# Kernel tuning notes

Measured on AMD Instinct MI355X. Metric: run time of the kernel, lower is better.

Reference implementation:

```python
import jax, jax.numpy as jnp
import numpy as np

T, B, D = 1024, 8, 1024
H, DH = 16, 64
EPS = 1e-12  # F.normalize eps

def _xavier(key, shape):
    fan_in, fan_out = shape[1], shape[0]
    a = float(np.sqrt(6.0 / (fan_in + fan_out)))
    return jax.random.uniform(key, shape, jnp.float32, -a, a)

def setup_inputs() -> dict:
    key = jax.random.key(0)
    ks = jax.random.split(key, 6)
    return {
        "x": jax.random.normal(ks[0], (T, B, D), jnp.float32),
        "S0": jnp.zeros((B, H, DH, DH), jnp.float32),
        "W_q": _xavier(ks[1], (D, D)),
        "W_k": _xavier(ks[2], (D, D)),
        "W_v": _xavier(ks[3], (D, D)),
        "W_alpha": _xavier(ks[4], (D, D)),
        "b_alpha": jnp.full((D,), 2.0, jnp.float32),
        "W_beta": _xavier(ks[5], (D, D)),
        "b_beta": jnp.zeros((D,), jnp.float32),
    }

def _l2norm(v):
    n = jnp.linalg.norm(v, axis=-1, keepdims=True)
    return v / jnp.maximum(n, EPS)

def reference(x, S0, W_q, W_k, W_v, W_alpha, b_alpha, W_beta, b_beta):
    t, b, d = x.shape
    h, dh = d // DH, DH
    xf = x.reshape(t * b, d)
    q = _l2norm((xf @ W_q.T).reshape(t, b, h, dh))
    k = _l2norm((xf @ W_k.T).reshape(t, b, h, dh))
    v = (xf @ W_v.T).reshape(t, b, h, dh)
    # per-head scalar gates: mean over head dim of sigmoid projections
    alpha = jax.nn.sigmoid(xf @ W_alpha.T + b_alpha).reshape(t, b, h, dh).mean(-1)  # [T,B,H]
    beta = jax.nn.sigmoid(xf @ W_beta.T + b_beta).reshape(t, b, h, dh).mean(-1)     # [T,B,H]

    def step(S, inp):
        qt, kt, vt, at, bt = inp  # [B,H,dh], [B,H,dh], [B,H,dh], [B,H], [B,H]
        a = at[:, :, None, None]
        be = bt[:, :, None, None]
        Sk = jnp.einsum('bhde,bhe->bhd', S, kt)                 # S @ k
        erase = Sk[..., :, None] * kt[..., None, :]             # (S k) k^T
        write = vt[..., :, None] * kt[..., None, :]             # v k^T
        S = a * (S - be * erase) + be * write
        out = jnp.einsum('bhde,bhe->bhd', S, qt).reshape(-1, d)  # [B,D]
        return S, out

    S_final, outs = jax.lax.scan(step, S0, (q, k, v, alpha, beta))
    return outs, S_final
```

## Files before the change

kernel.cpp:

```cpp
#include <hip/hip_runtime.h>
#include <hip/hip_bf16.h>
#include <math.h>

#define T_DIM 1024
#define B_DIM 8
#define D_DIM 1024
#define H_DIM 16
#define DH 64
#define M_ROWS 8192
#define N_COLS 5120
#define K_DIM 1024
#define PAD 72

typedef __attribute__((ext_vector_type(8))) short short8;
typedef __attribute__((ext_vector_type(4))) float floatx4;

static __device__ __forceinline__ unsigned short f2bf(float f){
    unsigned int u = __float_as_uint(f);
    u += 0x7fff + ((u >> 16) & 1);
    return (unsigned short)(u >> 16);
}
static __device__ __forceinline__ float sigf(float x){
    return 1.f / (1.f + __expf(-x));
}

#define DPPADD(x, ctrl) ((x) + __int_as_float(__builtin_amdgcn_update_dpp(0, __float_as_int(x), (ctrl), 0xF, 0xF, true)))
static __device__ __forceinline__ float red16(float x){
    x = DPPADD(x, 0xB1); x = DPPADD(x, 0x4E); x = DPPADD(x, 0x141); x = DPPADD(x, 0x140); return x;
}

__global__ void cvt_bf16(const float* __restrict__ src, unsigned short* __restrict__ dst, int n4){
    int i = blockIdx.x*blockDim.x + threadIdx.x;
    int stride = gridDim.x*blockDim.x;
    for (; i < n4; i += stride){
        float4 f = ((const float4*)src)[i];
        ushort4 o;
        o.x = f2bf(f.x); o.y = f2bf(f.y); o.z = f2bf(f.z); o.w = f2bf(f.w);
        ((ushort4*)dst)[i] = o;
    }
}

__global__ void cvt_w(const float* __restrict__ w0, const float* __restrict__ w1,
                      const float* __restrict__ w2, const float* __restrict__ w3,
                      const float* __restrict__ w4, unsigned short* __restrict__ dst){
    int i = blockIdx.x*blockDim.x + threadIdx.x;
    int seg = i >> 18;
    int off = i & 262143;
    const float* src = (seg==0)?w0:(seg==1)?w1:(seg==2)?w2:(seg==3)?w3:w4;
    float4 f = ((const float4*)src)[off];
    ushort4 o;
    o.x = f2bf(f.x); o.y = f2bf(f.y); o.z = f2bf(f.z); o.w = f2bf(f.w);
    ((ushort4*)dst)[i] = o;
}

#define GLD16(g, l) __builtin_amdgcn_global_load_lds(                         \
    (const __attribute__((address_space(1))) void*)(g),                       \
    (__attribute__((address_space(3))) void*)(l), 16, 0, 0)

#define SBAR() do { asm volatile("" ::: "memory"); __builtin_amdgcn_s_barrier(); asm volatile("" ::: "memory"); } while(0)

#define STAGE(slot, kk) do {                                                  \
    GLD16(pA0 + (kk)*32, &As[slot][tid*8]);                                   \
    GLD16(pA1 + (kk)*32, &As[slot][4096 + tid*8]);                            \
    GLD16(pB0 + (kk)*32, &Bs[slot][tid*8]);                                   \
    GLD16(pB1 + (kk)*32, &Bs[slot][4096 + tid*8]); } while(0)

#define READ_FRAGS(aF, bF, slot) do {                                         \
    aF[0] = *(const short8*)&As[slot][rowA];                                  \
    _Pragma("unroll")                                                         \
    for (int n = 0; n < 4; ++n) bF[n] = *(const short8*)&Bs[slot][rowB + n*512]; \
    _Pragma("unroll")                                                         \
    for (int m = 1; m < 8; ++m) aF[m] = *(const short8*)&As[slot][rowA + m*512]; \
} while(0)

#define MFMA_ALL(aF, bF) do {                                                 \
    __builtin_amdgcn_s_setprio(1);                                            \
    _Pragma("unroll")                                                         \
    for (int m = 0; m < 8; ++m)                                               \
        _Pragma("unroll")                                                     \
        for (int n = 0; n < 4; ++n)                                           \
            acc[m][n] = __builtin_amdgcn_mfma_f32_16x16x32_bf16(aF[m], bF[n], acc[m][n], 0,0,0); \
    __builtin_amdgcn_s_setprio(0);                                            \
} while(0)

__global__ __launch_bounds__(512, 2) void gemm_bt(const unsigned short* __restrict__ A,
                                                  const unsigned short* __restrict__ B,
                                                  unsigned char* __restrict__ KQV,
                                                  float* __restrict__ G,
                                                  const float* __restrict__ b_alpha,
                                                  const float* __restrict__ b_beta){
    __shared__ unsigned short As[4][8192];
    __shared__ unsigned short Bs[4][8192];
    const int tid = threadIdx.x;

    const int bid = blockIdx.y * 20 + blockIdx.x;
    const int xcd = bid & 7, idx = bid >> 3;
    const int ch = idx / 20, w20 = idx % 20;
    const int rowBase = (xcd*4 + (w20 & 3)) * 256;
    const int colBase = (ch*5 + (w20 >> 2)) * 256;

    const int l = tid & 63, l15 = l & 15, quad = l >> 4;
    const int wv = tid >> 6, wr = wv >> 2, wc = wv & 3;

    const int fk   = (quad ^ ((l15 >> 1) & 3)) * 8;
    const int rowA = (wr*128 + l15)*32 + fk;
    const int rowB = (wc*64  + l15)*32 + fk;

    const int kOff = ((tid & 3) ^ ((tid >> 3) & 3)) * 8;
    const unsigned short* pA0 = A + (size_t)(rowBase + (tid >> 2)) * K_DIM + kOff;
    const unsigned short* pA1 = pA0 + (size_t)128 * K_DIM;
    const unsigned short* pB0 = B + (size_t)(colBase + (tid >> 2)) * K_DIM + kOff;
    const unsigned short* pB1 = pB0 + (size_t)128 * K_DIM;

    floatx4 acc[8][4] = {};
    short8 aF0[8], bF0[4], aF1[8], bF1[4];

    STAGE(0, 0); STAGE(1, 1); STAGE(2, 2);
    asm volatile("s_waitcnt vmcnt(8)" ::: "memory");
    SBAR();
    READ_FRAGS(aF0, bF0, 0);
    asm volatile("s_waitcnt vmcnt(4)" ::: "memory");
    SBAR();

    for (int kk = 0; kk < 32; kk += 2){
        READ_FRAGS(aF1, bF1, (kk+1)&3);
        if (kk < 29) STAGE((kk+3)&3, kk+3);
        MFMA_ALL(aF0, bF0);
        if (kk < 29) asm volatile("s_waitcnt vmcnt(4)" ::: "memory");
        SBAR();
        if (kk+1 < 31) READ_FRAGS(aF0, bF0, (kk+2)&3);
        if (kk+1 < 29) STAGE((kk+4)&3, kk+4);
        MFMA_ALL(aF1, bF1);
        if (kk+1 < 29)       asm volatile("s_waitcnt vmcnt(4)" ::: "memory");
        else if (kk+1 == 29) asm volatile("s_waitcnt vmcnt(0)" ::: "memory");
        SBAR();
    }

    const int gcol = colBase + wc*64;
    const int seg  = gcol >> 10;
    const int rbw  = rowBase + wr*128 + quad*4;
    if (seg < 2){
        const int h = (gcol >> 6) & 15;
        const int segOff = (seg == 0) ? 128 : 0;
        #pragma unroll
        for (int m = 0; m < 8; ++m){
            #pragma unroll
            for (int r = 0; r < 4; ++r){
                float ss = acc[m][0][r]*acc[m][0][r] + acc[m][1][r]*acc[m][1][r]
                         + acc[m][2][r]*acc[m][2][r] + acc[m][3][r]*acc[m][3][r];
                ss = red16(ss);
                const float rn = 1.f / fmaxf(sqrtf(ss), 1e-12f);
                const int row = rbw + m*16 + r;
                const size_t rec = (size_t)((row & 7)*16 + h)*1024 + (row >> 3);
                unsigned short* rp = (unsigned short*)(KQV + rec*512 + segOff);
                #pragma unroll
                for (int n = 0; n < 4; ++n)
                    rp[n*16 + l15] = f2bf(acc[m][n][r] * rn);
            }
        }
    } else if (seg == 2){
        const int h = (gcol >> 6) & 15;
        #pragma unroll
        for (int m = 0; m < 8; ++m){
            #pragma unroll
            for (int r = 0; r < 4; ++r){
                const int row = rbw + m*16 + r;
                const size_t rec = (size_t)((row & 7)*16 + h)*1024 + (row >> 3);
                float* vp = (float*)(KQV + rec*512 + 256);
                #pragma unroll
                for (int n = 0; n < 4; ++n)
                    vp[n*16 + l15] = acc[m][n][r];
            }
        }
    } else {
        const int isBeta = (seg == 4) ? 1 : 0;
        const float* bias = isBeta ? b_beta : b_alpha;
        const int gcol0 = gcol - (isBeta ? 4096 : 3072);
        const int hh = gcol0 >> 6;
        float bj[4];
        #pragma unroll
        for (int n = 0; n < 4; ++n) bj[n] = bias[gcol0 + n*16 + l15];
        #pragma unroll
        for (int m = 0; m < 8; ++m){
            #pragma unroll
            for (int r = 0; r < 4; ++r){
                float sum = 0.f;
                #pragma unroll
                for (int n = 0; n < 4; ++n) sum += sigf(acc[m][n][r] + bj[n]);
                sum = red16(sum);
                if (l15 == 0){
                    const int row = rbw + m*16 + r;
                    const int tt = row >> 3, bb = row & 7;
                    G[(((size_t)(bb*16 + hh)*1024 + tt))*2 + isBeta] = sum * (1.f/64.f);
                }
            }
        }
    }
}

__global__ __launch_bounds__(256) void phasea(const unsigned char* __restrict__ KQV,
                                              const float* __restrict__ G,
                                              unsigned short* __restrict__ Wtg,
                                              unsigned short* __restrict__ Ng,
                                              float* __restrict__ rg){
    __shared__ unsigned short sKa[64*PAD], sQa[64*PAD];
    __shared__ float sAB[128];
    __shared__ float sKK[4096];
    __shared__ float sR[64], sRi[64];

    const int unitIdx = blockIdx.x;
    const int bh = unitIdx >> 4, c = unitIdx & 15;
    const int tid = threadIdx.x;
    const int w = tid>>6, l = tid&63, l15 = l&15, quad = l>>4;
    const unsigned char* gRec = KQV + ((size_t)bh*1024 + c*64)*512;

    #pragma unroll
    for (int it=0; it<2; ++it){
        int flat = it*256 + tid, t = flat>>3, i8 = flat&7;
        float4 kv = *(const float4*)(gRec + t*512 + i8*16);
        float4 qv = *(const float4*)(gRec + t*512 + 128 + i8*16);
        *(float4*)&sKa[t*PAD + i8*8] = kv;
        *(float4*)&sQa[t*PAD + i8*8] = qv;
    }
    if (tid < 64){
        float2 ab = *(const float2*)(G + ((size_t)bh*1024 + c*64 + tid)*2);
        sAB[tid*2] = ab.x; sAB[tid*2+1] = ab.y;
    }
    __syncthreads();
    if (tid < 64){
        float p = sAB[tid*2];
        #pragma unroll
        for (int off=1; off<64; off<<=1){
            float y = __shfl_up(p, off);
            if (tid >= off) p *= y;
        }
        sR[tid] = p; sRi[tid] = 1.f/p;
    }
    __syncthreads();

    {
        const int isQK = w >> 1;
        const int tmb = (w & 1)*2;
        floatx4 acc[2][4] = {};
        #pragma unroll
        for (int ks=0; ks<2; ++ks){
            short8 aA[2]; short8 bB[4];
            #pragma unroll
            for (int i=0;i<2;++i)
                aA[i] = *(const short8*)&((isQK? sQa : sKa)[((tmb+i)*16 + l15)*PAD + ks*32 + quad*8]);
            #pragma unroll
            for (int j2=0;j2<4;++j2)
                bB[j2] = *(const short8*)&sKa[(j2*16 + l15)*PAD + ks*32 + quad*8];
            #pragma unroll
            for (int i=0;i<2;++i)
                #pragma unroll
                for (int j2=0;j2<4;++j2)
                    acc[i][j2] = __builtin_amdgcn_mfma_f32_16x16x32_bf16(aA[i], bB[j2], acc[i][j2], 0,0,0);
        }
        #pragma unroll
        for (int i=0;i<2;++i){
            #pragma unroll
            for (int j2=0;j2<4;++j2){
                #pragma unroll
                for (int r=0;r<4;++r){
                    int t = (tmb+i)*16 + quad*4 + r;
                    int s = j2*16 + l15;
                    float ratio = sR[t]*sRi[s];
                    if (!isQK){
                        sKK[t*64+s] = (s < t) ? sAB[t*2+1]*ratio*acc[i][j2][r] : 0.f;
                    } else {
                        float nv = (s <= t) ? ratio*acc[i][j2][r] : 0.f;
                        Ng[(size_t)unitIdx*4096 + t*64 + s] = f2bf(nv);
                    }
                }
            }
        }
    }
    __syncthreads();

    if (tid < 64){
        const int s = tid;
        float X[64];
        X[0] = (s == 0) ? 1.f : 0.f;
        #pragma unroll
        for (int t=1; t<64; ++t){
            float a0 = 0.f, a1 = 0.f;
            const float* row = &sKK[t*64];
            int r = 0;
            #pragma unroll
            for (; r+4 <= t; r += 4){
                float4 cv = *(const float4*)&row[r];
                a0 += cv.x * X[r];
                a1 += cv.y * X[r+1];
                a0 += cv.z * X[r+2];
                a1 += cv.w * X[r+3];
            }
            #pragma unroll
            for (; r+1 < t; r += 2){
                a0 += row[r]   * X[r];
                a1 += row[r+1] * X[r+1];
            }
            if (r < t) a0 += row[r] * X[r];
            X[t] = (s == t) ? 1.f : -(a0+a1);
        }
        const float be = sAB[s*2+1];
        #pragma unroll
        for (int t=0; t<64; ++t)
            Wtg[(size_t)unitIdx*4096 + t*64 + s] = f2bf(X[t]*be);
        rg[(size_t)unitIdx*64 + s] = sR[s];
    }
}

__global__ __launch_bounds__(512) void chunk_scan(const unsigned char* __restrict__ KQV,
                                                  const unsigned short* __restrict__ Wtg,
                                                  const unsigned short* __restrict__ Ng,
                                                  const float* __restrict__ rg,
                                                  const float* __restrict__ S0g,
                                                  float* __restrict__ out){
    __shared__ unsigned short sK[64*PAD], sQ[64*PAD], sWt[64*PAD];
    __shared__ unsigned short sN[2][64*PAD];
    __shared__ unsigned short sUt[32*PAD];
    __shared__ unsigned short sKtU[64*PAD];
    __shared__ unsigned short sS0b[32*PAD];
    __shared__ float sr[2][64];

    const int bh = blockIdx.x & 127;
    const int half = blockIdx.x >> 7;
    const int b = bh >> 4, h = bh & 15;
    const int tid = threadIdx.x;
    const int w = tid >> 6, l = tid & 63, l15 = l & 15, quad = l >> 4;
    const int wt = w & 3, wg = w >> 2;
    const int t0 = wt*16 + quad*4;
    const int dq = wg*16;
    const int d2base = dq + quad*4;
    const unsigned char* gRec = KQV + (size_t)bh * (1024*512);
    const size_t outBase = (size_t)b*1024 + h*64 + half*32;

    float4 kst, qst, wst, nst;
    float rst = 0.f;
    float vCur[4], vNext[4];
    floatx4 Sreg;

    {
        const int unit = bh*16;
        const int t = tid>>3, i8 = tid&7;
        kst = *(const float4*)(gRec + t*512 +       i8*16);
        qst = *(const float4*)(gRec + t*512 + 128 + i8*16);
        wst = *(const float4*)((const unsigned char*)Wtg + (size_t)unit*8192 + (size_t)tid*16);
        nst = *(const float4*)((const unsigned char*)Ng  + (size_t)unit*8192 + (size_t)tid*16);
        if (tid < 64) rst = rg[(size_t)unit*64 + tid];
        #pragma unroll
        for (int r=0; r<4; ++r)
            vCur[r] = *(const float*)(gRec + (t0+r)*512 + 256 + (half*32 + dq + l15)*4);
        #pragma unroll
        for (int r=0;r<4;++r)
            Sreg[r] = S0g[(size_t)bh*4096 + (half*32 + d2base + r)*64 + wt*16 + l15];
        *(float4*)&sK[t*PAD + i8*8]    = kst;
        *(float4*)&sQ[t*PAD + i8*8]    = qst;
        *(float4*)&sWt[t*PAD + i8*8]   = wst;
        *(float4*)&sN[0][t*PAD + i8*8] = nst;
        if (tid < 64) sr[0][tid] = rst;
        #pragma unroll
        for (int r=0;r<4;++r)
            sS0b[(d2base+r)*PAD + wt*16 + l15] = f2bf(Sreg[r]);
    }
    __syncthreads();

    for (int c=0; c<16; ++c){
        const int buf = c & 1;
        if (c < 15){
            const int unit = bh*16 + c + 1;
            const unsigned char* gRecN = gRec + (size_t)(c+1)*64*512;
            const int t = tid>>3, i8 = tid&7;
            kst = *(const float4*)(gRecN + t*512 +       i8*16);
            qst = *(const float4*)(gRecN + t*512 + 128 + i8*16);
            wst = *(const float4*)((const unsigned char*)Wtg + (size_t)unit*8192 + (size_t)tid*16);
            nst = *(const float4*)((const unsigned char*)Ng  + (size_t)unit*8192 + (size_t)tid*16);
            if (tid < 64) rst = rg[(size_t)unit*64 + tid];
            #pragma unroll
            for (int r=0;r<4;++r)
                vNext[r] = *(const float*)(gRecN + (t0+r)*512 + 256 + (half*32 + dq + l15)*4);
        }

        floatx4 accPT = {}; floatx4 accOB = {};
        #pragma unroll
        for (int ks=0; ks<2; ++ks){
            short8 aK = *(const short8*)&sK[(wt*16 + l15)*PAD + ks*32 + quad*8];
            short8 aQ = *(const short8*)&sQ[(wt*16 + l15)*PAD + ks*32 + quad*8];
            short8 bS = *(const short8*)&sS0b[(dq + l15)*PAD + ks*32 + quad*8];
            accPT = __builtin_amdgcn_mfma_f32_16x16x32_bf16(aK, bS, accPT, 0,0,0);
            accOB = __builtin_amdgcn_mfma_f32_16x16x32_bf16(aQ, bS, accOB, 0,0,0);
        }
        float r4[4];
        #pragma unroll
        for (int r=0;r<4;++r) r4[r] = sr[buf][t0+r];
        {
            float x0 = vCur[0] - r4[0]*accPT[0];
            float x1 = vCur[1] - r4[1]*accPT[1];
            float x2 = vCur[2] - r4[2]*accPT[2];
            float x3 = vCur[3] - r4[3]*accPT[3];
            uint2 uu;
            uu.x = (unsigned)f2bf(x0) | ((unsigned)f2bf(x1)<<16);
            uu.y = (unsigned)f2bf(x2) | ((unsigned)f2bf(x3)<<16);
            *(uint2*)&sKtU[(dq + l15)*PAD + t0] = uu;
        }
        __syncthreads();

        floatx4 accU = {};
        #pragma unroll
        for (int ks=0; ks<2; ++ks){
            short8 aW = *(const short8*)&sWt[(wt*16 + l15)*PAD + ks*32 + quad*8];
            short8 bR = *(const short8*)&sKtU[(dq + l15)*PAD + ks*32 + quad*8];
            accU = __builtin_amdgcn_mfma_f32_16x16x32_bf16(aW, bR, accU, 0,0,0);
        }
        __syncthreads();

        {
            uint2 uu;
            uu.x = (unsigned)f2bf(accU[0]) | ((unsigned)f2bf(accU[1])<<16);
            uu.y = (unsigned)f2bf(accU[2]) | ((unsigned)f2bf(accU[3])<<16);
            *(uint2*)&sUt[(dq + l15)*PAD + t0] = uu;
        }
        {
            const float rl = sr[buf][63];
            const int e = tid >> 3, sb = (tid & 7)*8;
            #pragma unroll
            for (int j2=0; j2<8; ++j2){
                int s = sb + j2;
                float kv = __uint_as_float((unsigned)sK[s*PAD + e] << 16);
                sKtU[e*PAD + s] = f2bf(kv * (rl / sr[buf][s]));
            }
        }
        __syncthreads();

        floatx4 accO;
        #pragma unroll
        for (int r=0;r<4;++r) accO[r] = r4[r]*accOB[r];
        #pragma unroll
        for (int ks=0; ks<2; ++ks){
            short8 aN = *(const short8*)&sN[buf][(wt*16 + l15)*PAD + ks*32 + quad*8];
            short8 bU = *(const short8*)&sUt[(dq + l15)*PAD + ks*32 + quad*8];
            accO = __builtin_amdgcn_mfma_f32_16x16x32_bf16(aN, bU, accO, 0,0,0);
        }
        const float rl = sr[buf][63];
        floatx4 accS;
        #pragma unroll
        for (int r=0;r<4;++r) accS[r] = rl*Sreg[r];
        #pragma unroll
        for (int ks=0; ks<2; ++ks){
            short8 aU = *(const short8*)&sUt[(dq + l15)*PAD + ks*32 + quad*8];
            short8 bK = *(const short8*)&sKtU[(wt*16 + l15)*PAD + ks*32 + quad*8];
            accS = __builtin_amdgcn_mfma_f32_16x16x32_bf16(aU, bK, accS, 0,0,0);
        }
        Sreg = accS;

        #pragma unroll
        for (int r=0;r<4;++r)
            out[(size_t)(c*64 + t0 + r)*8192 + outBase + dq + l15] = accO[r];
        #pragma unroll
        for (int r=0;r<4;++r)
            sS0b[(d2base + r)*PAD + wt*16 + l15] = f2bf(Sreg[r]);

        if (c < 15){
            const int t = tid>>3, i8 = tid&7;
            *(float4*)&sK[t*PAD + i8*8]         = kst;
            *(float4*)&sQ[t*PAD + i8*8]         = qst;
            *(float4*)&sWt[t*PAD + i8*8]        = wst;
            *(float4*)&sN[buf^1][t*PAD + i8*8]  = nst;
            if (tid < 64) sr[buf^1][tid] = rst;
            #pragma unroll
            for (int r=0;r<4;++r) vCur[r] = vNext[r];
        }
        __syncthreads();
    }

    #pragma unroll
    for (int r=0;r<4;++r)
        out[(size_t)8388608 + (size_t)bh*4096 + (half*32 + d2base + r)*64 + wt*16 + l15] = Sreg[r];
}

extern "C" void kernel_launch(void* const* d_in, const int* in_sizes, int n_in,
                              void* d_out, int out_size, void* d_ws, size_t ws_size,
                              hipStream_t stream){
    const float* x  = (const float*)d_in[0];
    const float* S0 = (const float*)d_in[1];
    const float* Wq = (const float*)d_in[2];
    const float* Wk = (const float*)d_in[3];
    const float* Wv = (const float*)d_in[4];
    const float* Wa = (const float*)d_in[5];
    const float* ba = (const float*)d_in[6];
    const float* Wb = (const float*)d_in[7];
    const float* bb = (const float*)d_in[8];
    float* out = (float*)d_out;

    char* ws = (char*)d_ws;
    unsigned short* Abf = (unsigned short*)ws;
    unsigned short* Bbf = (unsigned short*)(ws + 16777216);
    unsigned char*  KQV = (unsigned char*) (ws + 27262976);
    float*          G   = (float*)         (ws + 94371840);
    unsigned short* Wtg = (unsigned short*)(ws + 95420416);
    unsigned short* Ng  = (unsigned short*)(ws + 112197632);
    float*          rg  = (float*)         (ws + 128974848);

    cvt_bf16<<<2048, 256, 0, stream>>>(x, Abf, (M_ROWS*K_DIM)/4);
    cvt_w<<<5120, 256, 0, stream>>>(Wq, Wk, Wv, Wa, Wb, Bbf);

    dim3 gg(N_COLS/256, M_ROWS/256);
    gemm_bt<<<gg, 512, 0, stream>>>(Abf, Bbf, KQV, G, ba, bb);

    phasea<<<2048, 256, 0, stream>>>(KQV, G, Wtg, Ng, rg);

    chunk_scan<<<256, 512, 0, stream>>>(KQV, Wtg, Ng, rg, S0, out);
}
```

Before: 282.5 us.

## Split chunk_scan value dimension into quarters across 512 smaller blocks

The chunked scan kernel now splits each (batch, head) state into four 16-row value slices instead of two 32-row halves. It launches 512 blocks of 256 threads rather than 256 blocks of 512, so more of the GPU's compute units have work during the sequential chunk loop. In exchange, each block redundantly loads and transposes the full K, Q, W and N chunk tiles. This doubles the global and LDS traffic for the shared operands per state element.

Result: slower. 324.1 us (+14.7%).

```diff
diff --git a/kernel.cpp b/kernel.cpp
--- a/kernel.cpp
+++ b/kernel.cpp
@@ -311,7 +311,7 @@
     }
 }
 
-__global__ __launch_bounds__(512) void chunk_scan(const unsigned char* __restrict__ KQV,
+__global__ __launch_bounds__(256) void chunk_scan(const unsigned char* __restrict__ KQV,
                                                   const unsigned short* __restrict__ Wtg,
                                                   const unsigned short* __restrict__ Ng,
                                                   const float* __restrict__ rg,
@@ -319,50 +319,56 @@
                                                   float* __restrict__ out){
     __shared__ unsigned short sK[64*PAD], sQ[64*PAD], sWt[64*PAD];
     __shared__ unsigned short sN[2][64*PAD];
-    __shared__ unsigned short sUt[32*PAD];
+    __shared__ unsigned short sUt[16*PAD];
     __shared__ unsigned short sKtU[64*PAD];
-    __shared__ unsigned short sS0b[32*PAD];
+    __shared__ unsigned short sS0b[16*PAD];
     __shared__ float sr[2][64];
 
     const int bh = blockIdx.x & 127;
-    const int half = blockIdx.x >> 7;
+    const int qtr = blockIdx.x >> 7;
     const int b = bh >> 4, h = bh & 15;
     const int tid = threadIdx.x;
     const int w = tid >> 6, l = tid & 63, l15 = l & 15, quad = l >> 4;
-    const int wt = w & 3, wg = w >> 2;
+    const int wt = w;
     const int t0 = wt*16 + quad*4;
-    const int dq = wg*16;
-    const int d2base = dq + quad*4;
+    const int dv0 = qtr*16;
     const unsigned char* gRec = KQV + (size_t)bh * (1024*512);
-    const size_t outBase = (size_t)b*1024 + h*64 + half*32;
-
-    float4 kst, qst, wst, nst;
+    const size_t outBase = (size_t)b*1024 + h*64 + dv0;
+
+    float4 kst[2], qst[2], wst[2], nst[2];
     float rst = 0.f;
     float vCur[4], vNext[4];
     floatx4 Sreg;
 
     {
         const int unit = bh*16;
-        const int t = tid>>3, i8 = tid&7;
-        kst = *(const float4*)(gRec + t*512 +       i8*16);
-        qst = *(const float4*)(gRec + t*512 + 128 + i8*16);
-        wst = *(const float4*)((const unsigned char*)Wtg + (size_t)unit*8192 + (size_t)tid*16);
-        nst = *(const float4*)((const unsigned char*)Ng  + (size_t)unit*8192 + (size_t)tid*16);
+        #pragma unroll
+        for (int it=0; it<2; ++it){
+            int flat = it*256 + tid, t = flat>>3, i8 = flat&7;
+            kst[it] = *(const float4*)(gRec + t*512 +       i8*16);
+            qst[it] = *(const float4*)(gRec + t*512 + 128 + i8*16);
+            wst[it] = *(const float4*)((const unsigned char*)Wtg + (size_t)unit*8192 + (size_t)flat*16);
+            nst[it] = *(const float4*)((const unsigned char*)Ng  + (size_t)unit*8192 + (size_t)flat*16);
+        }
         if (tid < 64) rst = rg[(size_t)unit*64 + tid];
         #pragma unroll
         for (int r=0; r<4; ++r)
-            vCur[r] = *(const float*)(gRec + (t0+r)*512 + 256 + (half*32 + dq + l15)*4);
+            vCur[r] = *(const float*)(gRec + (t0+r)*512 + 256 + (dv0 + l15)*4);
         #pragma unroll
         for (int r=0;r<4;++r)
-            Sreg[r] = S0g[(size_t)bh*4096 + (half*32 + d2base + r)*64 + wt*16 + l15];
-        *(float4*)&sK[t*PAD + i8*8]    = kst;
-        *(float4*)&sQ[t*PAD + i8*8]    = qst;
-        *(float4*)&sWt[t*PAD + i8*8]   = wst;
-        *(float4*)&sN[0][t*PAD + i8*8] = nst;
+            Sreg[r] = S0g[(size_t)bh*4096 + (dv0 + quad*4 + r)*64 + wt*16 + l15];
+        #pragma unroll
+        for (int it=0; it<2; ++it){
+            int flat = it*256 + tid, t = flat>>3, i8 = flat&7;
+            *(float4*)&sK[t*PAD + i8*8]    = kst[it];
+            *(float4*)&sQ[t*PAD + i8*8]    = qst[it];
+            *(float4*)&sWt[t*PAD + i8*8]   = wst[it];
+            *(float4*)&sN[0][t*PAD + i8*8] = nst[it];
+        }
         if (tid < 64) sr[0][tid] = rst;
         #pragma unroll
         for (int r=0;r<4;++r)
-            sS0b[(d2base+r)*PAD + wt*16 + l15] = f2bf(Sreg[r]);
+            sS0b[(quad*4+r)*PAD + wt*16 + l15] = f2bf(Sreg[r]);
     }
     __syncthreads();
 
@@ -371,15 +377,18 @@
         if (c < 15){
             const int unit = bh*16 + c + 1;
             const unsigned char* gRecN = gRec + (size_t)(c+1)*64*512;
-            const int t = tid>>3, i8 = tid&7;
-            kst = *(const float4*)(gRecN + t*512 +       i8*16);
-            qst = *(const float4*)(gRecN + t*512 + 128 + i8*16);
-            wst = *(const float4*)((const unsigned char*)Wtg + (size_t)unit*8192 + (size_t)tid*16);
-            nst = *(const float4*)((const unsigned char*)Ng  + (size_t)unit*8192 + (size_t)tid*16);
+            #pragma unroll
+            for (int it=0; it<2; ++it){
+                int flat = it*256 + tid, t = flat>>3, i8 = flat&7;
+                kst[it] = *(const float4*)(gRecN + t*512 +       i8*16);
+                qst[it] = *(const float4*)(gRecN + t*512 + 128 + i8*16);
+                wst[it] = *(const float4*)((const unsigned char*)Wtg + (size_t)unit*8192 + (size_t)flat*16);
+                nst[it] = *(const float4*)((const unsigned char*)Ng  + (size_t)unit*8192 + (size_t)flat*16);
+            }
             if (tid < 64) rst = rg[(size_t)unit*64 + tid];
             #pragma unroll
             for (int r=0;r<4;++r)
-                vNext[r] = *(const float*)(gRecN + (t0+r)*512 + 256 + (half*32 + dq + l15)*4);
+                vNext[r] = *(const float*)(gRecN + (t0+r)*512 + 256 + (dv0 + l15)*4);
         }
 
         floatx4 accPT = {}; floatx4 accOB = {};
@@ -387,7 +396,7 @@
         for (int ks=0; ks<2; ++ks){
             short8 aK = *(const short8*)&sK[(wt*16 + l15)*PAD + ks*32 + quad*8];
             short8 aQ = *(const short8*)&sQ[(wt*16 + l15)*PAD + ks*32 + quad*8];
-            short8 bS = *(const short8*)&sS0b[(dq + l15)*PAD + ks*32 + quad*8];
+            short8 bS = *(const short8*)&sS0b[l15*PAD + ks*32 + quad*8];
             accPT = __builtin_amdgcn_mfma_f32_16x16x32_bf16(aK, bS, accPT, 0,0,0);
             accOB = __builtin_amdgcn_mfma_f32_16x16x32_bf16(aQ, bS, accOB, 0,0,0);
         }
@@ -402,7 +411,7 @@
             uint2 uu;
             uu.x = (unsigned)f2bf(x0) | ((unsigned)f2bf(x1)<<16);
             uu.y = (unsigned)f2bf(x2) | ((unsigned)f2bf(x3)<<16);
-            *(uint2*)&sKtU[(dq + l15)*PAD + t0] = uu;
+            *(uint2*)&sKtU[l15*PAD + t0] = uu;
         }
         __syncthreads();
 
@@ -410,7 +419,7 @@
         #pragma unroll
         for (int ks=0; ks<2; ++ks){
             short8 aW = *(const short8*)&sWt[(wt*16 + l15)*PAD + ks*32 + quad*8];
-            short8 bR = *(const short8*)&sKtU[(dq + l15)*PAD + ks*32 + quad*8];
+            short8 bR = *(const short8*)&sKtU[l15*PAD + ks*32 + quad*8];
             accU = __builtin_amdgcn_mfma_f32_16x16x32_bf16(aW, bR, accU, 0,0,0);
         }
         __syncthreads();
@@ -419,13 +428,13 @@
             uint2 uu;
             uu.x = (unsigned)f2bf(accU[0]) | ((unsigned)f2bf(accU[1])<<16);
             uu.y = (unsigned)f2bf(accU[2]) | ((unsigned)f2bf(accU[3])<<16);
-            *(uint2*)&sUt[(dq + l15)*PAD + t0] = uu;
+            *(uint2*)&sUt[l15*PAD + t0] = uu;
         }
         {
             const float rl = sr[buf][63];
-            const int e = tid >> 3, sb = (tid & 7)*8;
-            #pragma unroll
-            for (int j2=0; j2<8; ++j2){
+            const int e = tid >> 2, sb = (tid & 3)*16;
+            #pragma unroll
+            for (int j2=0; j2<16; ++j2){
                 int s = sb + j2;
                 float kv = __uint_as_float((unsigned)sK[s*PAD + e] << 16);
                 sKtU[e*PAD + s] = f2bf(kv * (rl / sr[buf][s]));
@@ -439,7 +448,7 @@
         #pragma unroll
         for (int ks=0; ks<2; ++ks){
             short8 aN = *(const short8*)&sN[buf][(wt*16 + l15)*PAD + ks*32 + quad*8];
-            short8 bU = *(const short8*)&sUt[(dq + l15)*PAD + ks*32 + quad*8];
+            short8 bU = *(const short8*)&sUt[l15*PAD + ks*32 + quad*8];
             accO = __builtin_amdgcn_mfma_f32_16x16x32_bf16(aN, bU, accO, 0,0,0);
         }
         const float rl = sr[buf][63];
@@ -448,7 +457,7 @@
         for (int r=0;r<4;++r) accS[r] = rl*Sreg[r];
         #pragma unroll
         for (int ks=0; ks<2; ++ks){
-            short8 aU = *(const short8*)&sUt[(dq + l15)*PAD + ks*32 + quad*8];
+            short8 aU = *(const short8*)&sUt[l15*PAD + ks*32 + quad*8];
             short8 bK = *(const short8*)&sKtU[(wt*16 + l15)*PAD + ks*32 + quad*8];
             accS = __builtin_amdgcn_mfma_f32_16x16x32_bf16(aU, bK, accS, 0,0,0);
         }
@@ -456,17 +465,20 @@
 
         #pragma unroll
         for (int r=0;r<4;++r)
-            out[(size_t)(c*64 + t0 + r)*8192 + outBase + dq + l15] = accO[r];
+            out[(size_t)(c*64 + t0 + r)*8192 + outBase + l15] = accO[r];
         #pragma unroll
         for (int r=0;r<4;++r)
-            sS0b[(d2base + r)*PAD + wt*16 + l15] = f2bf(Sreg[r]);
+            sS0b[(quad*4 + r)*PAD + wt*16 + l15] = f2bf(Sreg[r]);
 
         if (c < 15){
-            const int t = tid>>3, i8 = tid&7;
-            *(float4*)&sK[t*PAD + i8*8]         = kst;
-            *(float4*)&sQ[t*PAD + i8*8]         = qst;
-            *(float4*)&sWt[t*PAD + i8*8]        = wst;
-            *(float4*)&sN[buf^1][t*PAD + i8*8]  = nst;
+            #pragma unroll
+            for (int it=0; it<2; ++it){
+                int flat = it*256 + tid, t = flat>>3, i8 = flat&7;
+                *(float4*)&sK[t*PAD + i8*8]         = kst[it];
+                *(float4*)&sQ[t*PAD + i8*8]         = qst[it];
+                *(float4*)&sWt[t*PAD + i8*8]        = wst[it];
+                *(float4*)&sN[buf^1][t*PAD + i8*8]  = nst[it];
+            }
             if (tid < 64) sr[buf^1][tid] = rst;
             #pragma unroll
             for (int r=0;r<4;++r) vCur[r] = vNext[r];
@@ -476,7 +488,7 @@
 
     #pragma unroll
     for (int r=0;r<4;++r)
-        out[(size_t)8388608 + (size_t)bh*4096 + (half*32 + d2base + r)*64 + wt*16 + l15] = Sreg[r];
+        out[(size_t)8388608 + (size_t)bh*4096 + (dv0 + quad*4 + r)*64 + wt*16 + l15] = Sreg[r];
 }
 
 extern "C" void kernel_launch(void* const* d_in, const int* in_sizes, int n_in,
@@ -510,5 +522,5 @@
 
     phasea<<<2048, 256, 0, stream>>>(KQV, G, Wtg, Ng, rg);
 
-    chunk_scan<<<256, 512, 0, stream>>>(KQV, Wtg, Ng, rg, S0, out);
-}
+    chunk_scan<<<512, 256, 0, stream>>>(KQV, Wtg, Ng, rg, S0, out);
+}
```
